# Performance work log

Measured on AMD Instinct MI355X. Metric: run time of the kernel, lower is better.

Reference implementation:

```python
import jax, jax.numpy as jnp
import numpy as np

B, L, D, H, A, NLAYERS, P = 16, 512, 768, 4, 100, 2, 3
DK = A // H  # 25
EPS = 1e-6


def setup_inputs() -> dict:
    key = jax.random.key(0)
    ks = jax.random.split(key, 20)
    s = 0.02
    return {
        "sequence_output": jax.random.normal(ks[0], (B, L, D), jnp.float32),
        "syntax_matrix": jax.random.normal(ks[1], (B, H, L, L), jnp.float32),
        # LayerNorm params
        "ln_a": jnp.ones((D,), jnp.float32),
        "ln_b": jnp.zeros((D,), jnp.float32),
        # Wxx: bert_dim -> attdim
        "Wxx_w": jax.random.normal(ks[2], (A, D), jnp.float32) * s,
        "Wxx_b": jnp.zeros((A,), jnp.float32),
        # attention q/k projections (attdim -> attdim)
        "q_w": jax.random.normal(ks[3], (A, A), jnp.float32) * s,
        "q_b": jnp.zeros((A,), jnp.float32),
        "k_w": jax.random.normal(ks[4], (A, A), jnp.float32) * s,
        "k_b": jnp.zeros((A,), jnp.float32),
        # W: attdim -> attdim
        "W_w": jax.random.normal(ks[5], (A, A), jnp.float32) * s,
        "W_b": jnp.zeros((A,), jnp.float32),
        # Wx: (H + 2*attdim) -> H
        "Wx_w": jax.random.normal(ks[6], (H, H + 2 * A), jnp.float32) * s,
        "Wx_b": jnp.zeros((H,), jnp.float32),
        # aggregate_W: attdim*(layers+1) -> attdim
        "agg_w": jax.random.normal(ks[7], (A, A * (NLAYERS + 1)), jnp.float32) * s,
        "agg_b": jnp.zeros((A,), jnp.float32),
        # classifier: 100 -> polarities_dim
        "cls_w": jax.random.normal(ks[8], (P, A), jnp.float32) * s,
        "cls_b": jnp.zeros((P,), jnp.float32),
        # masks (ints)
        "mask_ids": jnp.ones((B, L), jnp.int32),
        "src_mask": jnp.ones((B, L), jnp.int32),
    }


def reference(sequence_output, syntax_matrix, ln_a, ln_b, Wxx_w, Wxx_b,
              q_w, q_b, k_w, k_b, W_w, W_b, Wx_w, Wx_b,
              agg_w, agg_b, cls_w, cls_b, mask_ids, src_mask):
    # custom LayerNorm: torch.std is unbiased (ddof=1)
    mean = sequence_output.mean(-1, keepdims=True)
    std = jnp.std(sequence_output, axis=-1, ddof=1, keepdims=True)
    seq = ln_a * (sequence_output - mean) / (std + EPS) + ln_b

    # Wxx projection to attdim (dropout = identity in eval)
    x = seq @ Wxx_w.T + Wxx_b  # [B, L, A]

    # multi-head attention producing adjacency [B, H, L, L]
    q = (x @ q_w.T + q_b).reshape(B, L, H, DK).transpose(0, 2, 1, 3)
    k = (x @ k_w.T + k_b).reshape(B, L, H, DK).transpose(0, 2, 1, 3)
    scores = jnp.einsum('bhid,bhjd->bhij', q, k) / jnp.sqrt(jnp.float32(DK))
    key_mask = src_mask[:, None, None, :]  # [B,1,1,L]
    scores = jnp.where(key_mask == 0, jnp.float32(-1e9), scores)
    scores = scores + syntax_matrix
    adj = jax.nn.softmax(scores, axis=-1)  # [B, H, L, L]

    # split Wx into its adjacency / node-j / node-i blocks so the [B,L,L,H+2A]
    # concat tensor is never materialized (edge MLP is linear => decomposable)
    Aw = Wx_w[:, :H]            # [H, H]
    B1 = Wx_w[:, H:H + A]       # [H, A] applied to x[b, j]
    B2 = Wx_w[:, H + A:]        # [H, A] applied to x[b, i]

    x_g = x
    layer_list = [x]
    for i in range(NLAYERS):
        # Ax = mean over heads of adj_h @ x  (x identical per head)
        Ax = jnp.einsum('bhij,bjd->bid', adj, x_g) / H
        x_g = jax.nn.relu(Ax @ W_w.T + W_b)  # [B, L, A]
        layer_list.append(x_g)
        # edge update: edge[b,g,i,j] = sum_h Aw[g,h]*adj[b,h,i,j]
        e_adj = jnp.einsum('bhij,gh->bgij', adj, Aw)  # [B, H, L, L]
        u = jnp.einsum('bjd,gd->bgj', x_g, B1)        # node1 (index j)
        v = jnp.einsum('bid,gd->bgi', x_g, B2)        # node2 (index i)
        adj = e_adj + u[:, :, None, :] + v[:, :, :, None] + Wx_b[None, :, None, None]

    feats = jnp.concatenate(layer_list, axis=-1)          # [B, L, A*(NLAYERS+1)]
    node = jax.nn.relu(feats @ agg_w.T + agg_b)           # [B, L, A]

    valid_len = jnp.clip(mask_ids.sum(axis=1), 1, None).astype(node.dtype)[:, None]
    pooled = node.sum(axis=1) / valid_len                 # [B, A]
    logits = pooled @ cls_w.T + cls_b                     # [B, P]
    return logits
```

## Files before the change

### kernel.cpp

```cpp
#include <hip/hip_runtime.h>

#define B_ 16
#define L_ 512
#define D_ 768
#define H_ 4
#define A_ 100
#define DK_ 25
#define P_ 3
#define XP_ 128

__global__ __launch_bounds__(256) void k_prep(
    const float* __restrict__ Wxx_w, const float* __restrict__ agg_w,
    const float* __restrict__ q_w, const float* __restrict__ k_w,
    const float* __restrict__ W_w,
    float* __restrict__ wT, float* __restrict__ aggT,
    float* __restrict__ qkT, float* __restrict__ WT)
{
    int idx = blockIdx.x * 256 + threadIdx.x;
    if (idx < 98304) {
        const int d = idx >> 7, a = idx & 127;
        wT[idx] = (a < A_) ? Wxx_w[(size_t)a * D_ + d] : 0.f;
        return;
    }
    idx -= 98304;
    if (idx < 38400) {
        const int n = idx & 127, k = (idx >> 7) % A_, c = idx / (128 * A_);
        aggT[idx] = (n < A_) ? agg_w[(size_t)n * (3 * A_) + c * A_ + k] : 0.f;
        return;
    }
    idx -= 38400;
    if (idx < 25600) {
        const int n = idx & 255, k = idx >> 8;
        const int half = n >> 7, a = n & 127;
        const float* w = half ? k_w : q_w;
        qkT[idx] = (a < A_) ? w[(size_t)a * A_ + k] : 0.f;
        return;
    }
    idx -= 25600;
    if (idx < 12800) {
        const int n = idx & 127, k = idx >> 7;
        WT[idx] = (n < A_) ? W_w[(size_t)n * A_ + k] : 0.f;
    }
}

__global__ __launch_bounds__(256) void k_lnx(
    const float* __restrict__ seq, const float* __restrict__ ln_a, const float* __restrict__ ln_b,
    const float* __restrict__ wT, const float* __restrict__ Wxx_b, float* __restrict__ xp)
{
    __shared__ float ss[16][36];
    __shared__ float ws[32][128];
    __shared__ float mean_s[16], rd_s[16];
    const int tid = threadIdx.x;
    const int row0 = blockIdx.x * 16;
    const int wv = tid >> 6, lane = tid & 63;

    #pragma unroll
    for (int rr = 0; rr < 4; ++rr) {
        const int r = wv * 4 + rr;
        const float4* src = (const float4*)(seq + (size_t)(row0 + r) * D_);
        float4 a = src[lane], b = src[lane + 64], c = src[lane + 128];
        float s = a.x + a.y + a.z + a.w + b.x + b.y + b.z + b.w + c.x + c.y + c.z + c.w;
        #pragma unroll
        for (int o = 32; o; o >>= 1) s += __shfl_xor(s, o);
        const float m = s * (1.0f / 768.0f);
        float q = (a.x-m)*(a.x-m) + (a.y-m)*(a.y-m) + (a.z-m)*(a.z-m) + (a.w-m)*(a.w-m)
                + (b.x-m)*(b.x-m) + (b.y-m)*(b.y-m) + (b.z-m)*(b.z-m) + (b.w-m)*(b.w-m)
                + (c.x-m)*(c.x-m) + (c.y-m)*(c.y-m) + (c.z-m)*(c.z-m) + (c.w-m)*(c.w-m);
        #pragma unroll
        for (int o = 32; o; o >>= 1) q += __shfl_xor(q, o);
        if (lane == 0) {
            mean_s[r] = m;
            rd_s[r] = 1.0f / (sqrtf(q * (1.0f / 767.0f)) + 1e-6f);
        }
    }
    __syncthreads();

    const int c4 = tid & 31, rowg = tid >> 5;
    float4 acc0 = {0.f, 0.f, 0.f, 0.f};
    float4 acc1 = {0.f, 0.f, 0.f, 0.f};

    for (int kc = 0; kc < 24; ++kc) {
        if (tid < 128) {
            const int r = tid >> 3, k4 = tid & 7;
            float4 v = *(const float4*)(seq + (size_t)(row0 + r) * D_ + kc * 32 + k4 * 4);
            float4 la = ((const float4*)ln_a)[kc * 8 + k4];
            float4 lb = ((const float4*)ln_b)[kc * 8 + k4];
            const float m = mean_s[r], rd = rd_s[r];
            float4 o;
            o.x = la.x * ((v.x - m) * rd) + lb.x;
            o.y = la.y * ((v.y - m) * rd) + lb.y;
            o.z = la.z * ((v.z - m) * rd) + lb.z;
            o.w = la.w * ((v.w - m) * rd) + lb.w;
            *(float4*)&ss[r][k4 * 4] = o;
        }
        #pragma unroll
        for (int t = 0; t < 4; ++t) {
            const int idx = tid + t * 256;
            const int k = idx >> 5, cc = idx & 31;
            *(float4*)&ws[k][cc * 4] = *(const float4*)(wT + (size_t)(kc * 32 + k) * 128 + cc * 4);
        }
        __syncthreads();
        #pragma unroll 4
        for (int k = 0; k < 32; k += 4) {
            float4 sv0 = *(float4*)&ss[rowg * 2 + 0][k];
            float4 sv1 = *(float4*)&ss[rowg * 2 + 1][k];
            #pragma unroll
            for (int j = 0; j < 4; ++j) {
                float4 w4 = *(float4*)&ws[k + j][c4 * 4];
                const float s0 = ((float*)&sv0)[j];
                const float s1 = ((float*)&sv1)[j];
                acc0.x += s0 * w4.x; acc0.y += s0 * w4.y;
                acc0.z += s0 * w4.z; acc0.w += s0 * w4.w;
                acc1.x += s1 * w4.x; acc1.y += s1 * w4.y;
                acc1.z += s1 * w4.z; acc1.w += s1 * w4.w;
            }
        }
        __syncthreads();
    }

    float4 bias = {0.f, 0.f, 0.f, 0.f};
    if (c4 < 25) bias = ((const float4*)Wxx_b)[c4];
    float4 o0, o1;
    o0.x = acc0.x + bias.x; o0.y = acc0.y + bias.y;
    o0.z = acc0.z + bias.z; o0.w = acc0.w + bias.w;
    o1.x = acc1.x + bias.x; o1.y = acc1.y + bias.y;
    o1.z = acc1.z + bias.z; o1.w = acc1.w + bias.w;
    *(float4*)(xp + (size_t)(row0 + rowg * 2 + 0) * XP_ + c4 * 4) = o0;
    *(float4*)(xp + (size_t)(row0 + rowg * 2 + 1) * XP_ + c4 * 4) = o1;
}

__global__ __launch_bounds__(256) void k_qkg(
    const float* __restrict__ xp, const float* __restrict__ qkT,
    const float* __restrict__ q_b, const float* __restrict__ k_b,
    float* __restrict__ qt, float* __restrict__ kt)
{
    __shared__ float ss[32][104];
    __shared__ float ws[A_][128];
    const int tid = threadIdx.x;
    const int row0 = blockIdx.x * 32;
    const int half = blockIdx.y;
    const int c4 = tid & 31, rg = tid >> 5;

    for (int idx = tid; idx < 32 * 25; idx += 256) {
        const int r = idx / 25, k4 = idx % 25;
        *(float4*)&ss[r][k4 * 4] = *(const float4*)(xp + (size_t)(row0 + r) * XP_ + k4 * 4);
    }
    for (int idx = tid; idx < A_ * 32; idx += 256) {
        const int k = idx >> 5, cc = idx & 31;
        *(float4*)&ws[k][cc * 4] = *(const float4*)(qkT + (size_t)k * 256 + half * 128 + cc * 4);
    }
    __syncthreads();

    float4 acc[4];
    #pragma unroll
    for (int i = 0; i < 4; ++i) { acc[i].x = acc[i].y = acc[i].z = acc[i].w = 0.f; }
    #pragma unroll 5
    for (int k = 0; k < A_; k += 4) {
        float4 sv[4];
        #pragma unroll
        for (int i = 0; i < 4; ++i) sv[i] = *(float4*)&ss[rg * 4 + i][k];
        #pragma unroll
        for (int j = 0; j < 4; ++j) {
            float4 w4 = *(float4*)&ws[k + j][c4 * 4];
            #pragma unroll
            for (int i = 0; i < 4; ++i) {
                const float sj = ((float*)&sv[i])[j];
                acc[i].x += sj * w4.x; acc[i].y += sj * w4.y;
                acc[i].z += sj * w4.z; acc[i].w += sj * w4.w;
            }
        }
    }

    if (c4 < 25) {
        const float4 bias = ((const float4*)(half ? k_b : q_b))[c4];
        float* dst = half ? kt : qt;
        #pragma unroll
        for (int i = 0; i < 4; ++i) {
            float4 o;
            o.x = acc[i].x + bias.x; o.y = acc[i].y + bias.y;
            o.z = acc[i].z + bias.z; o.w = acc[i].w + bias.w;
            *(float4*)(dst + (size_t)(row0 + rg * 4 + i) * A_ + c4 * 4) = o;
        }
    }
}

__global__ __launch_bounds__(256) void k_sgemm(
    const float* __restrict__ qt, const float* __restrict__ kt,
    const float* __restrict__ syn, const int* __restrict__ src_mask,
    float* __restrict__ es)
{
    __shared__ float qs[DK_][64];
    __shared__ float ks[DK_][64];
    __shared__ int ms[64];
    const int tid = threadIdx.x;
    const int bh = blockIdx.z;
    const int b = bh >> 2, h = bh & 3;
    const int i0 = blockIdx.x * 64, j0 = blockIdx.y * 64;
    const float* qbase = qt + ((size_t)b * L_ + i0) * A_ + h * DK_;
    const float* kbase = kt + ((size_t)b * L_ + j0) * A_ + h * DK_;
    {
        const int r = tid >> 2, c = tid & 3;
        #pragma unroll
        for (int k = 0; k < 7; ++k) {
            const int d = c + 4 * k;
            if (d < DK_) {
                qs[d][r] = qbase[(size_t)r * A_ + d];
                ks[d][r] = kbase[(size_t)r * A_ + d];
            }
        }
        if (tid < 64) ms[tid] = src_mask[b * L_ + j0 + tid];
    }
    __syncthreads();
    const int ty = tid >> 4, tx = tid & 15;
    float acc[4][4] = {};
    #pragma unroll 5
    for (int d = 0; d < DK_; ++d) {
        float4 qv = *(const float4*)&qs[d][ty * 4];
        float4 kv = *(const float4*)&ks[d][tx * 4];
        const float q[4] = {qv.x, qv.y, qv.z, qv.w};
        const float kk[4] = {kv.x, kv.y, kv.z, kv.w};
        #pragma unroll
        for (int ii = 0; ii < 4; ++ii)
            #pragma unroll
            for (int jj = 0; jj < 4; ++jj)
                acc[ii][jj] += q[ii] * kk[jj];
    }
    const int irow = i0 + ty * 4, jcol = j0 + tx * 4;
    const int m0 = ms[tx * 4], m1 = ms[tx * 4 + 1], m2 = ms[tx * 4 + 2], m3 = ms[tx * 4 + 3];
    #pragma unroll
    for (int ii = 0; ii < 4; ++ii) {
        const size_t o = ((size_t)bh * L_ + irow + ii) * L_ + jcol;
        float4 sv = *(const float4*)(syn + o);
        float4 w;
        w.x = (m0 ? acc[ii][0] * 0.2f : -1e9f) + sv.x;
        w.y = (m1 ? acc[ii][1] * 0.2f : -1e9f) + sv.y;
        w.z = (m2 ? acc[ii][2] * 0.2f : -1e9f) + sv.z;
        w.w = (m3 ? acc[ii][3] * 0.2f : -1e9f) + sv.w;
        *(float4*)(es + o) = w;
    }
}

__global__ __launch_bounds__(256) void k_softmax(
    const float* __restrict__ Wx_w, float* __restrict__ es)
{
    __shared__ float ps[H_][L_];
    __shared__ float cs[H_];
    const int tid = threadIdx.x, r = blockIdx.x;
    const int b = r >> 9, i = r & 511;
    const int h = tid >> 6, lane = tid & 63;
    if (tid < H_) cs[tid] = Wx_w[tid] + Wx_w[204 + tid] + Wx_w[408 + tid] + Wx_w[612 + tid];
    float* row = es + (((size_t)(b * H_ + h)) * L_ + i) * L_;
    float4 v0 = ((const float4*)row)[lane];
    float4 v1 = ((const float4*)row)[lane + 64];
    float mx = fmaxf(fmaxf(fmaxf(v0.x, v0.y), fmaxf(v0.z, v0.w)),
                     fmaxf(fmaxf(v1.x, v1.y), fmaxf(v1.z, v1.w)));
    #pragma unroll
    for (int o = 32; o; o >>= 1) mx = fmaxf(mx, __shfl_xor(mx, o));
    float4 e0, e1;
    e0.x = __expf(v0.x - mx); e0.y = __expf(v0.y - mx);
    e0.z = __expf(v0.z - mx); e0.w = __expf(v0.w - mx);
    e1.x = __expf(v1.x - mx); e1.y = __expf(v1.y - mx);
    e1.z = __expf(v1.z - mx); e1.w = __expf(v1.w - mx);
    float sum = e0.x + e0.y + e0.z + e0.w + e1.x + e1.y + e1.z + e1.w;
    #pragma unroll
    for (int o = 32; o; o >>= 1) sum += __shfl_xor(sum, o);
    const float inv = 1.0f / sum;
    e0.x *= inv; e0.y *= inv; e0.z *= inv; e0.w *= inv;
    e1.x *= inv; e1.y *= inv; e1.z *= inv; e1.w *= inv;
    *(float4*)&ps[h][lane * 4] = e0;
    *(float4*)&ps[h][(lane + 64) * 4] = e1;
    __syncthreads();
    float* arow = es + (((size_t)(b * H_ + 0)) * L_ + i) * L_;
    float* wrow = es + (((size_t)(b * H_ + 1)) * L_ + i) * L_;
    const int t = tid & 127;
    float4 p0 = *(float4*)&ps[0][t * 4];
    float4 p1 = *(float4*)&ps[1][t * 4];
    float4 p2 = *(float4*)&ps[2][t * 4];
    float4 p3 = *(float4*)&ps[3][t * 4];
    if (tid < 128) {
        float4 o;
        o.x = p0.x + p1.x + p2.x + p3.x;
        o.y = p0.y + p1.y + p2.y + p3.y;
        o.z = p0.z + p1.z + p2.z + p3.z;
        o.w = p0.w + p1.w + p2.w + p3.w;
        *(float4*)(arow + t * 4) = o;
    } else {
        const float c0 = cs[0], c1 = cs[1], c2 = cs[2], c3 = cs[3];
        float4 o;
        o.x = c0 * p0.x + c1 * p1.x + c2 * p2.x + c3 * p3.x;
        o.y = c0 * p0.y + c1 * p1.y + c2 * p2.y + c3 * p3.y;
        o.z = c0 * p0.z + c1 * p1.z + c2 * p2.z + c3 * p3.z;
        o.w = c0 * p0.w + c1 * p1.w + c2 * p2.w + c3 * p3.w;
        *(float4*)(wrow + t * 4) = o;
    }
}

template<int LAYER2>
__global__ __launch_bounds__(256) void k_axg(
    const float* __restrict__ adj, const float* __restrict__ xp,
    const float* __restrict__ S, const float* __restrict__ T,
    const float* __restrict__ Vv, const float* __restrict__ Wx_b,
    float* __restrict__ axb)
{
    __shared__ float ss[16][36];
    __shared__ float ws[32][128];
    const int tid = threadIdx.x;
    const int row0 = blockIdx.x * 16;
    const int b = row0 >> 9, i0 = row0 & 511;
    const float* adjb = adj + (size_t)b * 4 * L_ * L_;
    const int c4 = tid & 31, rowg = tid >> 5;
    float4 acc0 = {0.f, 0.f, 0.f, 0.f};
    float4 acc1 = {0.f, 0.f, 0.f, 0.f};

    for (int kc = 0; kc < 16; ++kc) {
        if (tid < 128) {
            const int r = tid >> 3, q4 = tid & 7;
            *(float4*)&ss[r][q4 * 4] =
                *(const float4*)(adjb + (size_t)(i0 + r) * L_ + kc * 32 + q4 * 4);
        }
        #pragma unroll
        for (int t = 0; t < 4; ++t) {
            const int idx = tid + t * 256;
            const int k = idx >> 5, cc = idx & 31;
            *(float4*)&ws[k][cc * 4] =
                *(const float4*)(xp + ((size_t)b * L_ + kc * 32 + k) * XP_ + cc * 4);
        }
        __syncthreads();
        #pragma unroll 4
        for (int k = 0; k < 32; k += 4) {
            float4 sv0 = *(float4*)&ss[rowg * 2 + 0][k];
            float4 sv1 = *(float4*)&ss[rowg * 2 + 1][k];
            #pragma unroll
            for (int j = 0; j < 4; ++j) {
                float4 w4 = *(float4*)&ws[k + j][c4 * 4];
                const float s0 = ((float*)&sv0)[j];
                const float s1 = ((float*)&sv1)[j];
                acc0.x += s0 * w4.x; acc0.y += s0 * w4.y;
                acc0.z += s0 * w4.z; acc0.w += s0 * w4.w;
                acc1.x += s1 * w4.x; acc1.y += s1 * w4.y;
                acc1.z += s1 * w4.z; acc1.w += s1 * w4.w;
            }
        }
        __syncthreads();
    }

    float wb = 0.f;
    float4 Sv = {0.f, 0.f, 0.f, 0.f}, Tv = {0.f, 0.f, 0.f, 0.f};
    if (LAYER2) {
        wb = Wx_b[0] + Wx_b[1] + Wx_b[2] + Wx_b[3];
        if (c4 < 25) {
            Sv = ((const float4*)(S + b * A_))[c4];
            Tv = ((const float4*)(T + b * A_))[c4];
        }
    }
    const int grow0 = row0 + rowg * 2;
    const float vv0 = LAYER2 ? (Vv[grow0] + wb) : 0.f;
    const float vv1 = LAYER2 ? (Vv[grow0 + 1] + wb) : 0.f;
    float4 o0, o1;
    o0.x = (acc0.x + Sv.x + vv0 * Tv.x) * 0.25f;
    o0.y = (acc0.y + Sv.y + vv0 * Tv.y) * 0.25f;
    o0.z = (acc0.z + Sv.z + vv0 * Tv.z) * 0.25f;
    o0.w = (acc0.w + Sv.w + vv0 * Tv.w) * 0.25f;
    o1.x = (acc1.x + Sv.x + vv1 * Tv.x) * 0.25f;
    o1.y = (acc1.y + Sv.y + vv1 * Tv.y) * 0.25f;
    o1.z = (acc1.z + Sv.z + vv1 * Tv.z) * 0.25f;
    o1.w = (acc1.w + Sv.w + vv1 * Tv.w) * 0.25f;
    *(float4*)(axb + (size_t)grow0 * XP_ + c4 * 4) = o0;
    *(float4*)(axb + (size_t)(grow0 + 1) * XP_ + c4 * 4) = o1;
}

__global__ __launch_bounds__(256) void k_xw(
    const float* __restrict__ axb, const float* __restrict__ WT,
    const float* __restrict__ W_b, float* __restrict__ xout)
{
    __shared__ float ss[32][104];
    __shared__ float ws[A_][128];
    const int tid = threadIdx.x;
    const int row0 = blockIdx.x * 32;
    const int c4 = tid & 31, rg = tid >> 5;

    for (int idx = tid; idx < 32 * 25; idx += 256) {
        const int r = idx / 25, k4 = idx % 25;
        *(float4*)&ss[r][k4 * 4] = *(const float4*)(axb + (size_t)(row0 + r) * XP_ + k4 * 4);
    }
    for (int idx = tid; idx < A_ * 32; idx += 256) {
        const int k = idx >> 5, cc = idx & 31;
        *(float4*)&ws[k][cc * 4] = *(const float4*)(WT + (size_t)k * 128 + cc * 4);
    }
    __syncthreads();

    float4 acc[4];
    #pragma unroll
    for (int i = 0; i < 4; ++i) { acc[i].x = acc[i].y = acc[i].z = acc[i].w = 0.f; }
    #pragma unroll 5
    for (int k = 0; k < A_; k += 4) {
        float4 sv[4];
        #pragma unroll
        for (int i = 0; i < 4; ++i) sv[i] = *(float4*)&ss[rg * 4 + i][k];
        #pragma unroll
        for (int j = 0; j < 4; ++j) {
            float4 w4 = *(float4*)&ws[k + j][c4 * 4];
            #pragma unroll
            for (int i = 0; i < 4; ++i) {
                const float sj = ((float*)&sv[i])[j];
                acc[i].x += sj * w4.x; acc[i].y += sj * w4.y;
                acc[i].z += sj * w4.z; acc[i].w += sj * w4.w;
            }
        }
    }

    float4 bias = {0.f, 0.f, 0.f, 0.f};
    if (c4 < 25) bias = ((const float4*)W_b)[c4];
    #pragma unroll
    for (int i = 0; i < 4; ++i) {
        float4 o;
        o.x = fmaxf(acc[i].x + bias.x, 0.f); o.y = fmaxf(acc[i].y + bias.y, 0.f);
        o.z = fmaxf(acc[i].z + bias.z, 0.f); o.w = fmaxf(acc[i].w + bias.w, 0.f);
        *(float4*)(xout + (size_t)(row0 + rg * 4 + i) * XP_ + c4 * 4) = o;
    }
}

__global__ __launch_bounds__(256) void k_extras(
    const float* __restrict__ x1, const float* __restrict__ Wx_w,
    float* __restrict__ Vv, float* __restrict__ T, float* __restrict__ S,
    float* __restrict__ pooled)
{
    __shared__ float b1s[A_], b2s[A_], Ul[L_];
    const int tid = threadIdx.x, b = blockIdx.x;
    if (tid < A_) {
        float s1 = 0.f, s2 = 0.f;
        #pragma unroll
        for (int g = 0; g < H_; ++g) {
            s1 += Wx_w[g * 204 + 4 + tid];
            s2 += Wx_w[g * 204 + 104 + tid];
        }
        b1s[tid] = s1; b2s[tid] = s2;
        pooled[b * A_ + tid] = 0.f;
    }
    __syncthreads();
    for (int j = tid; j < L_; j += 256) {
        const float* xr = x1 + ((size_t)b * L_ + j) * XP_;
        float u = 0.f, v = 0.f;
        #pragma unroll 4
        for (int c = 0; c < A_; ++c) { float xv = xr[c]; u += xv * b1s[c]; v += xv * b2s[c]; }
        Ul[j] = u;
        Vv[b * L_ + j] = v;
    }
    __syncthreads();
    if (tid < A_) {
        float t = 0.f, s = 0.f;
        for (int j = 0; j < L_; ++j) {
            float xv = x1[((size_t)b * L_ + j) * XP_ + tid];
            t += xv; s += Ul[j] * xv;
        }
        T[b * A_ + tid] = t; S[b * A_ + tid] = s;
    }
}

__global__ __launch_bounds__(256) void k_nodepool(
    const float* __restrict__ x, const float* __restrict__ x1, const float* __restrict__ x2,
    const float* __restrict__ aggT, const float* __restrict__ agg_b,
    float* __restrict__ pooled)
{
    __shared__ float ss[32][104];
    __shared__ float ws[A_][128];
    const int tid = threadIdx.x;
    const int row0 = blockIdx.x * 32;
    const int b = row0 >> 9;
    const int c4 = tid & 31, rg = tid >> 5;
    float4 acc[4];
    #pragma unroll
    for (int i = 0; i < 4; ++i) { acc[i].x = acc[i].y = acc[i].z = acc[i].w = 0.f; }

    for (int c = 0; c < 3; ++c) {
        const float* src = (c == 0) ? x : (c == 1) ? x1 : x2;
        for (int idx = tid; idx < 32 * 25; idx += 256) {
            const int r = idx / 25, k4 = idx % 25;
            *(float4*)&ss[r][k4 * 4] =
                *(const float4*)(src + (size_t)(row0 + r) * XP_ + k4 * 4);
        }
        for (int idx = tid; idx < A_ * 32; idx += 256) {
            const int k = idx >> 5, cc = idx & 31;
            *(float4*)&ws[k][cc * 4] =
                *(const float4*)(aggT + ((size_t)c * A_ + k) * 128 + cc * 4);
        }
        __syncthreads();
        #pragma unroll 5
        for (int k = 0; k < A_; k += 4) {
            float4 sv[4];
            #pragma unroll
            for (int i = 0; i < 4; ++i) sv[i] = *(float4*)&ss[rg * 4 + i][k];
            #pragma unroll
            for (int j = 0; j < 4; ++j) {
                float4 w4 = *(float4*)&ws[k + j][c4 * 4];
                #pragma unroll
                for (int i = 0; i < 4; ++i) {
                    const float sj = ((float*)&sv[i])[j];
                    acc[i].x += sj * w4.x; acc[i].y += sj * w4.y;
                    acc[i].z += sj * w4.z; acc[i].w += sj * w4.w;
                }
            }
        }
        __syncthreads();
    }

    float4 bias = {0.f, 0.f, 0.f, 0.f};
    if (c4 < 25) bias = ((const float4*)agg_b)[c4];
    float4 rs = {0.f, 0.f, 0.f, 0.f};
    #pragma unroll
    for (int i = 0; i < 4; ++i) {
        rs.x += fmaxf(acc[i].x + bias.x, 0.f);
        rs.y += fmaxf(acc[i].y + bias.y, 0.f);
        rs.z += fmaxf(acc[i].z + bias.z, 0.f);
        rs.w += fmaxf(acc[i].w + bias.w, 0.f);
    }
    float* red = &ss[0][0];
    __syncthreads();
    *(float4*)&red[rg * 128 + c4 * 4] = rs;
    __syncthreads();
    if (rg == 0 && c4 < 25) {
        float4 tot = {0.f, 0.f, 0.f, 0.f};
        #pragma unroll
        for (int g = 0; g < 8; ++g) {
            float4 v = *(float4*)&red[g * 128 + c4 * 4];
            tot.x += v.x; tot.y += v.y; tot.z += v.z; tot.w += v.w;
        }
        atomicAdd(&pooled[b * A_ + c4 * 4 + 0], tot.x);
        atomicAdd(&pooled[b * A_ + c4 * 4 + 1], tot.y);
        atomicAdd(&pooled[b * A_ + c4 * 4 + 2], tot.z);
        atomicAdd(&pooled[b * A_ + c4 * 4 + 3], tot.w);
    }
}

__global__ __launch_bounds__(64) void k_logits(
    const float* __restrict__ pooled, const float* __restrict__ cls_w,
    const float* __restrict__ cls_b, const int* __restrict__ mask_ids,
    float* __restrict__ out)
{
    const int tid = threadIdx.x;
    if (tid < B_ * P_) {
        const int b = tid / P_, p = tid % P_;
        int vs = 0;
        for (int l = 0; l < L_; ++l) vs += mask_ids[b * L_ + l];
        float inv = 1.0f / (float)max(vs, 1);
        float acc = cls_b[p];
        #pragma unroll 4
        for (int a = 0; a < A_; ++a) acc += (pooled[b * A_ + a] * inv) * cls_w[p * A_ + a];
        out[b * P_ + p] = acc;
    }
}

extern "C" void kernel_launch(void* const* d_in, const int* in_sizes, int n_in,
                              void* d_out, int out_size, void* d_ws, size_t ws_size,
                              hipStream_t stream) {
    const float* seq    = (const float*)d_in[0];
    const float* syn    = (const float*)d_in[1];
    const float* ln_a   = (const float*)d_in[2];
    const float* ln_b   = (const float*)d_in[3];
    const float* Wxx_w  = (const float*)d_in[4];
    const float* Wxx_b  = (const float*)d_in[5];
    const float* q_w    = (const float*)d_in[6];
    const float* q_b    = (const float*)d_in[7];
    const float* k_w    = (const float*)d_in[8];
    const float* k_b    = (const float*)d_in[9];
    const float* W_w    = (const float*)d_in[10];
    const float* W_b    = (const float*)d_in[11];
    const float* Wx_w   = (const float*)d_in[12];
    const float* Wx_b   = (const float*)d_in[13];
    const float* agg_w  = (const float*)d_in[14];
    const float* agg_b  = (const float*)d_in[15];
    const float* cls_w  = (const float*)d_in[16];
    const float* cls_b  = (const float*)d_in[17];
    const int* mask_ids = (const int*)d_in[18];
    const int* src_mask = (const int*)d_in[19];
    float* out = (float*)d_out;

    float* ws = (float*)d_ws;
    size_t off = 0;
    float* xp     = ws + off; off += (size_t)B_ * L_ * XP_;
    float* x1p    = ws + off; off += (size_t)B_ * L_ * XP_;
    float* x2p    = ws + off; off += (size_t)B_ * L_ * XP_;
    float* axb    = ws + off; off += (size_t)B_ * L_ * XP_;
    float* qt     = ws + off; off += (size_t)B_ * L_ * A_;
    float* kt     = ws + off; off += (size_t)B_ * L_ * A_;
    float* es     = ws + off; off += (size_t)B_ * H_ * L_ * L_;
    float* Vv     = ws + off; off += (size_t)B_ * L_;
    float* T      = ws + off; off += (size_t)B_ * A_;
    float* S      = ws + off; off += (size_t)B_ * A_;
    float* pooled = ws + off; off += (size_t)B_ * A_;
    float* wT     = ws + off; off += (size_t)D_ * 128;
    float* aggT   = ws + off; off += (size_t)3 * A_ * 128;
    float* qkT    = ws + off; off += (size_t)A_ * 256;
    float* WT     = ws + off; off += (size_t)A_ * 128;

    k_prep<<<(98304 + 38400 + 25600 + 12800 + 255) / 256, 256, 0, stream>>>(
        Wxx_w, agg_w, q_w, k_w, W_w, wT, aggT, qkT, WT);
    k_lnx<<<(B_ * L_) / 16, 256, 0, stream>>>(seq, ln_a, ln_b, wT, Wxx_b, xp);
    k_qkg<<<dim3((B_ * L_) / 32, 2), 256, 0, stream>>>(xp, qkT, q_b, k_b, qt, kt);
    k_sgemm<<<dim3(8, 8, B_ * H_), 256, 0, stream>>>(qt, kt, syn, src_mask, es);
    k_softmax<<<B_ * L_, 256, 0, stream>>>(Wx_w, es);
    k_axg<0><<<(B_ * L_) / 16, 256, 0, stream>>>(es, xp, nullptr, nullptr, nullptr, nullptr, axb);
    k_xw<<<(B_ * L_) / 32, 256, 0, stream>>>(axb, WT, W_b, x1p);
    k_extras<<<B_, 256, 0, stream>>>(x1p, Wx_w, Vv, T, S, pooled);
    k_axg<1><<<(B_ * L_) / 16, 256, 0, stream>>>(es + (size_t)L_ * L_, x1p, S, T, Vv, Wx_b, axb);
    k_xw<<<(B_ * L_) / 32, 256, 0, stream>>>(axb, WT, W_b, x2p);
    k_nodepool<<<(B_ * L_) / 32, 256, 0, stream>>>(xp, x1p, x2p, aggT, agg_b, pooled);
    k_logits<<<1, 64, 0, stream>>>(pooled, cls_w, cls_b, mask_ids, out);
}
```

Baseline: 383.6 us.

## Fold LayerNorm into Wxx weights and double-buffer GEMM tiles in lnx/axg

LayerNorm scale and shift are folded algebraically into the Wxx projection. Prep now produces ln_a-scaled weights plus two per-column vectors (u = ln_a·W and vb = ln_b·W + bias), so k_lnx multiplies raw inputs and applies the mean and rstd correction in the epilogue. Both k_lnx and k_axg switch to double-buffered shared-memory tiles with register prefetch, so the next K-chunk's global loads overlap compute and only one barrier is needed per iteration. Shared memory per block doubles, which may reduce occupancy. The folded form computes sum(w·x) − mean·sum(w), which can cancel precision when the mean is large.

```diff
diff --git a/kernel.cpp b/kernel.cpp
--- a/kernel.cpp
+++ b/kernel.cpp
@@ -12,14 +12,16 @@
 __global__ __launch_bounds__(256) void k_prep(
     const float* __restrict__ Wxx_w, const float* __restrict__ agg_w,
     const float* __restrict__ q_w, const float* __restrict__ k_w,
-    const float* __restrict__ W_w,
-    float* __restrict__ wT, float* __restrict__ aggT,
-    float* __restrict__ qkT, float* __restrict__ WT)
+    const float* __restrict__ W_w, const float* __restrict__ ln_a,
+    const float* __restrict__ ln_b, const float* __restrict__ Wxx_b,
+    float* __restrict__ wT2, float* __restrict__ aggT,
+    float* __restrict__ qkT, float* __restrict__ WT,
+    float* __restrict__ u_, float* __restrict__ vb_)
 {
     int idx = blockIdx.x * 256 + threadIdx.x;
     if (idx < 98304) {
         const int d = idx >> 7, a = idx & 127;
-        wT[idx] = (a < A_) ? Wxx_w[(size_t)a * D_ + d] : 0.f;
+        wT2[idx] = (a < A_) ? ln_a[d] * Wxx_w[(size_t)a * D_ + d] : 0.f;
         return;
     }
     idx -= 98304;
@@ -40,15 +42,30 @@
     if (idx < 12800) {
         const int n = idx & 127, k = idx >> 7;
         WT[idx] = (n < A_) ? W_w[(size_t)n * A_ + k] : 0.f;
+        return;
+    }
+    idx -= 12800;
+    if (idx < 128) {
+        float uu = 0.f, vv = 0.f;
+        if (idx < A_) {
+            for (int d = 0; d < D_; ++d) {
+                const float w = Wxx_w[(size_t)idx * D_ + d];
+                uu += ln_a[d] * w;
+                vv += ln_b[d] * w;
+            }
+            vv += Wxx_b[idx];
+        }
+        u_[idx] = uu; vb_[idx] = vv;
     }
 }
 
 __global__ __launch_bounds__(256) void k_lnx(
-    const float* __restrict__ seq, const float* __restrict__ ln_a, const float* __restrict__ ln_b,
-    const float* __restrict__ wT, const float* __restrict__ Wxx_b, float* __restrict__ xp)
-{
-    __shared__ float ss[16][36];
-    __shared__ float ws[32][128];
+    const float* __restrict__ seq, const float* __restrict__ wT2,
+    const float* __restrict__ u_, const float* __restrict__ vb_,
+    float* __restrict__ xp)
+{
+    __shared__ float ss[2][16][36];
+    __shared__ float ws[2][32][128];
     __shared__ float mean_s[16], rd_s[16];
     const int tid = threadIdx.x;
     const int row0 = blockIdx.x * 16;
@@ -73,40 +90,48 @@
             rd_s[r] = 1.0f / (sqrtf(q * (1.0f / 767.0f)) + 1e-6f);
         }
     }
+
+    const int sr = tid >> 3, sk4 = tid & 7;
+    float4 rs = {0.f, 0.f, 0.f, 0.f};
+    float4 rw[4];
+
+    if (tid < 128)
+        rs = *(const float4*)(seq + (size_t)(row0 + sr) * D_ + sk4 * 4);
+    #pragma unroll
+    for (int t = 0; t < 4; ++t) {
+        const int idx = tid + t * 256;
+        rw[t] = *(const float4*)(wT2 + (size_t)(idx >> 5) * 128 + (idx & 31) * 4);
+    }
+    if (tid < 128) *(float4*)&ss[0][sr][sk4 * 4] = rs;
+    #pragma unroll
+    for (int t = 0; t < 4; ++t) {
+        const int idx = tid + t * 256;
+        *(float4*)&ws[0][idx >> 5][(idx & 31) * 4] = rw[t];
+    }
     __syncthreads();
 
     const int c4 = tid & 31, rowg = tid >> 5;
     float4 acc0 = {0.f, 0.f, 0.f, 0.f};
     float4 acc1 = {0.f, 0.f, 0.f, 0.f};
+    int cur = 0;
 
     for (int kc = 0; kc < 24; ++kc) {
-        if (tid < 128) {
-            const int r = tid >> 3, k4 = tid & 7;
-            float4 v = *(const float4*)(seq + (size_t)(row0 + r) * D_ + kc * 32 + k4 * 4);
-            float4 la = ((const float4*)ln_a)[kc * 8 + k4];
-            float4 lb = ((const float4*)ln_b)[kc * 8 + k4];
-            const float m = mean_s[r], rd = rd_s[r];
-            float4 o;
-            o.x = la.x * ((v.x - m) * rd) + lb.x;
-            o.y = la.y * ((v.y - m) * rd) + lb.y;
-            o.z = la.z * ((v.z - m) * rd) + lb.z;
-            o.w = la.w * ((v.w - m) * rd) + lb.w;
-            *(float4*)&ss[r][k4 * 4] = o;
-        }
-        #pragma unroll
-        for (int t = 0; t < 4; ++t) {
-            const int idx = tid + t * 256;
-            const int k = idx >> 5, cc = idx & 31;
-            *(float4*)&ws[k][cc * 4] = *(const float4*)(wT + (size_t)(kc * 32 + k) * 128 + cc * 4);
-        }
-        __syncthreads();
+        if (kc < 23) {
+            if (tid < 128)
+                rs = *(const float4*)(seq + (size_t)(row0 + sr) * D_ + (kc + 1) * 32 + sk4 * 4);
+            #pragma unroll
+            for (int t = 0; t < 4; ++t) {
+                const int idx = tid + t * 256;
+                rw[t] = *(const float4*)(wT2 + (size_t)((kc + 1) * 32 + (idx >> 5)) * 128 + (idx & 31) * 4);
+            }
+        }
         #pragma unroll 4
         for (int k = 0; k < 32; k += 4) {
-            float4 sv0 = *(float4*)&ss[rowg * 2 + 0][k];
-            float4 sv1 = *(float4*)&ss[rowg * 2 + 1][k];
+            float4 sv0 = *(float4*)&ss[cur][rowg * 2 + 0][k];
+            float4 sv1 = *(float4*)&ss[cur][rowg * 2 + 1][k];
             #pragma unroll
             for (int j = 0; j < 4; ++j) {
-                float4 w4 = *(float4*)&ws[k + j][c4 * 4];
+                float4 w4 = *(float4*)&ws[cur][k + j][c4 * 4];
                 const float s0 = ((float*)&sv0)[j];
                 const float s1 = ((float*)&sv1)[j];
                 acc0.x += s0 * w4.x; acc0.y += s0 * w4.y;
@@ -115,16 +140,31 @@
                 acc1.z += s1 * w4.z; acc1.w += s1 * w4.w;
             }
         }
+        if (kc < 23) {
+            if (tid < 128) *(float4*)&ss[cur ^ 1][sr][sk4 * 4] = rs;
+            #pragma unroll
+            for (int t = 0; t < 4; ++t) {
+                const int idx = tid + t * 256;
+                *(float4*)&ws[cur ^ 1][idx >> 5][(idx & 31) * 4] = rw[t];
+            }
+        }
         __syncthreads();
-    }
-
-    float4 bias = {0.f, 0.f, 0.f, 0.f};
-    if (c4 < 25) bias = ((const float4*)Wxx_b)[c4];
+        cur ^= 1;
+    }
+
+    const float m0 = mean_s[rowg * 2 + 0], rd0 = rd_s[rowg * 2 + 0];
+    const float m1 = mean_s[rowg * 2 + 1], rd1 = rd_s[rowg * 2 + 1];
+    const float4 uu = ((const float4*)u_)[c4];
+    const float4 vv = ((const float4*)vb_)[c4];
     float4 o0, o1;
-    o0.x = acc0.x + bias.x; o0.y = acc0.y + bias.y;
-    o0.z = acc0.z + bias.z; o0.w = acc0.w + bias.w;
-    o1.x = acc1.x + bias.x; o1.y = acc1.y + bias.y;
-    o1.z = acc1.z + bias.z; o1.w = acc1.w + bias.w;
+    o0.x = rd0 * acc0.x - rd0 * m0 * uu.x + vv.x;
+    o0.y = rd0 * acc0.y - rd0 * m0 * uu.y + vv.y;
+    o0.z = rd0 * acc0.z - rd0 * m0 * uu.z + vv.z;
+    o0.w = rd0 * acc0.w - rd0 * m0 * uu.w + vv.w;
+    o1.x = rd1 * acc1.x - rd1 * m1 * uu.x + vv.x;
+    o1.y = rd1 * acc1.y - rd1 * m1 * uu.y + vv.y;
+    o1.z = rd1 * acc1.z - rd1 * m1 * uu.z + vv.z;
+    o1.w = rd1 * acc1.w - rd1 * m1 * uu.w + vv.w;
     *(float4*)(xp + (size_t)(row0 + rowg * 2 + 0) * XP_ + c4 * 4) = o0;
     *(float4*)(xp + (size_t)(row0 + rowg * 2 + 1) * XP_ + c4 * 4) = o1;
 }
@@ -302,37 +342,54 @@
     const float* __restrict__ Vv, const float* __restrict__ Wx_b,
     float* __restrict__ axb)
 {
-    __shared__ float ss[16][36];
-    __shared__ float ws[32][128];
+    __shared__ float ss[2][16][36];
+    __shared__ float ws[2][32][128];
     const int tid = threadIdx.x;
     const int row0 = blockIdx.x * 16;
     const int b = row0 >> 9, i0 = row0 & 511;
     const float* adjb = adj + (size_t)b * 4 * L_ * L_;
     const int c4 = tid & 31, rowg = tid >> 5;
+
+    const int sr = tid >> 3, sk4 = tid & 7;
+    float4 rs = {0.f, 0.f, 0.f, 0.f};
+    float4 rw[4];
+
+    if (tid < 128)
+        rs = *(const float4*)(adjb + (size_t)(i0 + sr) * L_ + sk4 * 4);
+    #pragma unroll
+    for (int t = 0; t < 4; ++t) {
+        const int idx = tid + t * 256;
+        rw[t] = *(const float4*)(xp + ((size_t)b * L_ + (idx >> 5)) * XP_ + (idx & 31) * 4);
+    }
+    if (tid < 128) *(float4*)&ss[0][sr][sk4 * 4] = rs;
+    #pragma unroll
+    for (int t = 0; t < 4; ++t) {
+        const int idx = tid + t * 256;
+        *(float4*)&ws[0][idx >> 5][(idx & 31) * 4] = rw[t];
+    }
+    __syncthreads();
+
     float4 acc0 = {0.f, 0.f, 0.f, 0.f};
     float4 acc1 = {0.f, 0.f, 0.f, 0.f};
+    int cur = 0;
 
     for (int kc = 0; kc < 16; ++kc) {
-        if (tid < 128) {
-            const int r = tid >> 3, q4 = tid & 7;
-            *(float4*)&ss[r][q4 * 4] =
-                *(const float4*)(adjb + (size_t)(i0 + r) * L_ + kc * 32 + q4 * 4);
-        }
-        #pragma unroll
-        for (int t = 0; t < 4; ++t) {
-            const int idx = tid + t * 256;
-            const int k = idx >> 5, cc = idx & 31;
-            *(float4*)&ws[k][cc * 4] =
-                *(const float4*)(xp + ((size_t)b * L_ + kc * 32 + k) * XP_ + cc * 4);
-        }
-        __syncthreads();
+        if (kc < 15) {
+            if (tid < 128)
+                rs = *(const float4*)(adjb + (size_t)(i0 + sr) * L_ + (kc + 1) * 32 + sk4 * 4);
+            #pragma unroll
+            for (int t = 0; t < 4; ++t) {
+                const int idx = tid + t * 256;
+                rw[t] = *(const float4*)(xp + ((size_t)b * L_ + (kc + 1) * 32 + (idx >> 5)) * XP_ + (idx & 31) * 4);
+            }
+        }
         #pragma unroll 4
         for (int k = 0; k < 32; k += 4) {
-            float4 sv0 = *(float4*)&ss[rowg * 2 + 0][k];
-            float4 sv1 = *(float4*)&ss[rowg * 2 + 1][k];
+            float4 sv0 = *(float4*)&ss[cur][rowg * 2 + 0][k];
+            float4 sv1 = *(float4*)&ss[cur][rowg * 2 + 1][k];
             #pragma unroll
             for (int j = 0; j < 4; ++j) {
-                float4 w4 = *(float4*)&ws[k + j][c4 * 4];
+                float4 w4 = *(float4*)&ws[cur][k + j][c4 * 4];
                 const float s0 = ((float*)&sv0)[j];
                 const float s1 = ((float*)&sv1)[j];
                 acc0.x += s0 * w4.x; acc0.y += s0 * w4.y;
@@ -341,7 +398,16 @@
                 acc1.z += s1 * w4.z; acc1.w += s1 * w4.w;
             }
         }
+        if (kc < 15) {
+            if (tid < 128) *(float4*)&ss[cur ^ 1][sr][sk4 * 4] = rs;
+            #pragma unroll
+            for (int t = 0; t < 4; ++t) {
+                const int idx = tid + t * 256;
+                *(float4*)&ws[cur ^ 1][idx >> 5][(idx & 31) * 4] = rw[t];
+            }
+        }
         __syncthreads();
+        cur ^= 1;
     }
 
     float wb = 0.f;
@@ -588,14 +654,16 @@
     float* T      = ws + off; off += (size_t)B_ * A_;
     float* S      = ws + off; off += (size_t)B_ * A_;
     float* pooled = ws + off; off += (size_t)B_ * A_;
-    float* wT     = ws + off; off += (size_t)D_ * 128;
+    float* wT2    = ws + off; off += (size_t)D_ * 128;
     float* aggT   = ws + off; off += (size_t)3 * A_ * 128;
     float* qkT    = ws + off; off += (size_t)A_ * 256;
     float* WT     = ws + off; off += (size_t)A_ * 128;
-
-    k_prep<<<(98304 + 38400 + 25600 + 12800 + 255) / 256, 256, 0, stream>>>(
-        Wxx_w, agg_w, q_w, k_w, W_w, wT, aggT, qkT, WT);
-    k_lnx<<<(B_ * L_) / 16, 256, 0, stream>>>(seq, ln_a, ln_b, wT, Wxx_b, xp);
+    float* u_     = ws + off; off += 128;
+    float* vb_    = ws + off; off += 128;
+
+    k_prep<<<(98304 + 38400 + 25600 + 12800 + 128 + 255) / 256, 256, 0, stream>>>(
+        Wxx_w, agg_w, q_w, k_w, W_w, ln_a, ln_b, Wxx_b, wT2, aggT, qkT, WT, u_, vb_);
+    k_lnx<<<(B_ * L_) / 16, 256, 0, stream>>>(seq, wT2, u_, vb_, xp);
     k_qkg<<<dim3((B_ * L_) / 32, 2), 256, 0, stream>>>(xp, qkT, q_b, k_b, qt, kt);
     k_sgemm<<<dim3(8, 8, B_ * H_), 256, 0, stream>>>(qt, kt, syn, src_mask, es);
     k_softmax<<<B_ * L_, 256, 0, stream>>>(Wx_w, es);
```

Measured after the change: 443.5 us. +15.6%, slower.
